# Performance work log

Measured on AMD Instinct MI355X. Metric: run time of the kernel, lower is better.

The kernel has to match this reference:

```python
import jax, jax.numpy as jnp
import numpy as np

D_MODEL = 1024
N_HEAD = 16
B, S = 2, 2048


def setup_inputs() -> dict:
    key = jax.random.key(0)
    ks = jax.random.split(key, 12)
    scale = 1.0 / np.sqrt(D_MODEL)
    inp = {
        "q": jax.random.normal(ks[0], (B, S, D_MODEL), jnp.float32),
        "k": jax.random.normal(ks[1], (B, S, D_MODEL), jnp.float32),
        "v": jax.random.normal(ks[2], (B, S, D_MODEL), jnp.float32),
        "mask": jax.random.randint(ks[3], (B, S, S), 0, 2, jnp.int32),
        "Wq": jax.random.normal(ks[4], (D_MODEL, D_MODEL), jnp.float32) * scale,
        "bq": jnp.zeros((D_MODEL,), jnp.float32),
        "Wk": jax.random.normal(ks[5], (D_MODEL, D_MODEL), jnp.float32) * scale,
        "bk": jnp.zeros((D_MODEL,), jnp.float32),
        "Wv": jax.random.normal(ks[6], (D_MODEL, D_MODEL), jnp.float32) * scale,
        "bv": jnp.zeros((D_MODEL,), jnp.float32),
        "Wo": jax.random.normal(ks[7], (D_MODEL, D_MODEL), jnp.float32) * scale,
        "bo": jnp.zeros((D_MODEL,), jnp.float32),
    }
    return inp


def reference(q, k, v, mask, Wq, bq, Wk, bk, Wv, bv, Wo, bo):
    b, s, d = q.shape
    dh = d // N_HEAD

    def proj_split(x, W, bias):
        # torch nn.Linear: x @ W.T + b; then split to [b, h, s, dh]
        y = x @ W.T + bias
        return y.reshape(b, s, N_HEAD, dh).transpose(0, 2, 1, 3)

    qh = proj_split(q, Wq, bq)
    kh = proj_split(k, Wk, bk)
    vh = proj_split(v, Wv, bv)

    # score: [b, h, s_q, s_k]
    score = jnp.einsum("bhqd,bhkd->bhqk", qh, kh) / jnp.sqrt(jnp.float32(dh))
    score = jnp.where(mask[:, None, :, :] == 0, jnp.float32(-10000.0), score)
    attn = jax.nn.softmax(score, axis=-1)

    out = jnp.einsum("bhqk,bhkd->bhqd", attn, vh)
    out = out.transpose(0, 2, 1, 3).reshape(b, s, d)
    return out @ Wo.T + bo
```

## Files before the change

### kernel.cpp

```cpp
#include <hip/hip_runtime.h>

typedef unsigned short u16;
typedef __bf16 bf16x8 __attribute__((ext_vector_type(8)));
typedef float f32x4 __attribute__((ext_vector_type(4)));

#define D_MODEL 1024
#define NH 16
#define DH 64
#define BB 2
#define SS 2048

#if __has_builtin(__builtin_amdgcn_exp2f)
#define EXP2f(x) __builtin_amdgcn_exp2f(x)
#else
#define EXP2f(x) exp2f(x)
#endif

__device__ __forceinline__ u16 f2bf_fast(float f) {
    union { float f; unsigned int u; } v; v.f = f;
    return (u16)((v.u + 0x8000u) >> 16);
}
__device__ __forceinline__ uint4 pack8(const float4& a, const float4& b) {
    unsigned int a0 = __float_as_uint(a.x) + 0x8000u, a1 = __float_as_uint(a.y) + 0x8000u;
    unsigned int a2 = __float_as_uint(a.z) + 0x8000u, a3 = __float_as_uint(a.w) + 0x8000u;
    unsigned int b0 = __float_as_uint(b.x) + 0x8000u, b1 = __float_as_uint(b.y) + 0x8000u;
    unsigned int b2 = __float_as_uint(b.z) + 0x8000u, b3 = __float_as_uint(b.w) + 0x8000u;
    uint4 r;
    r.x = __builtin_amdgcn_perm(a1, a0, 0x07060302);
    r.y = __builtin_amdgcn_perm(a3, a2, 0x07060302);
    r.z = __builtin_amdgcn_perm(b1, b0, 0x07060302);
    r.w = __builtin_amdgcn_perm(b3, b2, 0x07060302);
    return r;
}

__device__ __forceinline__ void gld16(const void* g, void* l) {
    __builtin_amdgcn_global_load_lds(
        (const __attribute__((address_space(1))) unsigned int*)g,
        (__attribute__((address_space(3))) unsigned int*)l, 16, 0, 0);
}

__global__ __launch_bounds__(256) void cvtw_kernel(
    const float* __restrict__ Wq, const float* __restrict__ Wk,
    const float* __restrict__ Wv, const float* __restrict__ Wo, u16* __restrict__ cW)
{
    int z = blockIdx.y;
    const float* src = (z == 0) ? Wq : (z == 1) ? Wk : (z == 2) ? Wv : Wo;
    u16* dst = cW + (size_t)z * D_MODEL * D_MODEL;
    size_t base = ((size_t)blockIdx.x * 256 + threadIdx.x) * 8;
    float4 a = *reinterpret_cast<const float4*>(src + base);
    float4 b = *reinterpret_cast<const float4*>(src + base + 4);
    *reinterpret_cast<uint4*>(dst + base) = pack8(a, b);
}

__global__ __launch_bounds__(256) void cvtin_kernel(
    const float* __restrict__ q, const float* __restrict__ k,
    const float* __restrict__ v, u16* __restrict__ qb)
{
    int z = blockIdx.y;
    const float* src = (z == 0) ? q : (z == 1) ? k : v;
    u16* dst = qb + (size_t)z * BB * SS * D_MODEL;
    size_t base = ((size_t)blockIdx.x * 256 + threadIdx.x) * 8;
    float4 a = *reinterpret_cast<const float4*>(src + base);
    float4 b = *reinterpret_cast<const float4*>(src + base + 4);
    *reinterpret_cast<uint4*>(dst + base) = pack8(a, b);
}

__global__ __launch_bounds__(256) void maskpack_kernel(
    const int* __restrict__ mask, unsigned long long* __restrict__ pm)
{
    int gw = (blockIdx.x * 256 + threadIdx.x) >> 6;
    int l = threadIdx.x & 63;
#pragma unroll 4
    for (int i = 0; i < 32; ++i) {
        int widx = gw * 32 + i;
        int m = mask[(size_t)widx * 64 + l];
        unsigned long long bits = __ballot(m != 0);
        if (l == 0) pm[widx] = bits;
    }
}

template<int OF32, int QKV>
__device__ void gemm_bb(const u16* __restrict__ A, const u16* __restrict__ W,
                        const float* __restrict__ bias, void* outp, float oscale)
{
    __shared__ __align__(16) u16 smem[128 * 144];
    u16* lA = smem;
    u16* lW = smem + 128 * 64;
    const int t = threadIdx.x, w = t >> 6, l = t & 63;
    const int blockM = blockIdx.x * 128, blockN = blockIdx.y * 128;
    const int lrow = l >> 3, lcol = (l & 7) * 8;
    const int quad = l >> 4, c16 = l & 15;

    f32x4 acc[4][4] = {};

    for (int kt = 0; kt < 16; ++kt) {
        __syncthreads();
#pragma unroll
        for (int i = 0; i < 4; ++i) {
            int c = w * 4 + i;
            int row = c * 8 + lrow;
            gld16(A + (size_t)(blockM + row) * 1024 + kt * 64 + lcol, &lA[c * 512]);
            gld16(W + (size_t)(blockN + row) * 1024 + kt * 64 + lcol, &lW[c * 512]);
        }
        __syncthreads();
#pragma unroll
        for (int ks = 0; ks < 2; ++ks) {
            bf16x8 af[4], bfr[4];
#pragma unroll
            for (int mi = 0; mi < 4; ++mi)
                af[mi] = *reinterpret_cast<const bf16x8*>(
                    &lA[((w & 1) * 64 + mi * 16 + c16) * 64 + ks * 32 + quad * 8]);
#pragma unroll
            for (int ni = 0; ni < 4; ++ni)
                bfr[ni] = *reinterpret_cast<const bf16x8*>(
                    &lW[((w >> 1) * 64 + ni * 16 + c16) * 64 + ks * 32 + quad * 8]);
#pragma unroll
            for (int mi = 0; mi < 4; ++mi)
#pragma unroll
                for (int ni = 0; ni < 4; ++ni)
                    acc[mi][ni] = __builtin_amdgcn_mfma_f32_16x16x32_bf16(
                        af[mi], bfr[ni], acc[mi][ni], 0, 0, 0);
        }
    }

    if (QKV) {
        __syncthreads();
        const int m_base = (w & 1) * 64, n_base = (w >> 1) * 64;
#pragma unroll
        for (int ni = 0; ni < 4; ++ni) {
            int n_local = n_base + ni * 16 + c16;
            float bv = bias[blockN + n_local];
#pragma unroll
            for (int mi = 0; mi < 4; ++mi)
#pragma unroll
                for (int r = 0; r < 4; ++r) {
                    int m_local = m_base + mi * 16 + quad * 4 + r;
                    smem[m_local * 136 + n_local] =
                        f2bf_fast((acc[mi][ni][r] + bv) * oscale);
                }
        }
        __syncthreads();
        const int bb = blockM >> 11, s_base = blockM & 2047;
        u16* outb = (u16*)outp;
#pragma unroll
        for (int i = 0; i < 8; ++i) {
            int idx = t + i * 256;
            int mrow = idx >> 4, ch = idx & 15;
            uint4 val = *reinterpret_cast<const uint4*>(&smem[mrow * 136 + ch * 8]);
            int gn = blockN + ch * 8;
            int hh = gn >> 6, dh = gn & 63;
            *reinterpret_cast<uint4*>(
                outb + (((size_t)(bb * NH + hh)) * SS + s_base + mrow) * DH + dh) = val;
        }
        return;
    }

    const int m0 = blockM + (w & 1) * 64, n0 = blockN + (w >> 1) * 64;
#pragma unroll
    for (int ni = 0; ni < 4; ++ni) {
        int n = n0 + ni * 16 + c16;
        float bv = bias[n];
#pragma unroll
        for (int mi = 0; mi < 4; ++mi) {
#pragma unroll
            for (int r = 0; r < 4; ++r) {
                int m = m0 + mi * 16 + quad * 4 + r;
                float val = (acc[mi][ni][r] + bv) * oscale;
                ((float*)outp)[(size_t)m * 1024 + n] = val;
            }
        }
    }
}

__global__ __launch_bounds__(256) void qkv_kernel(
    const u16* __restrict__ qb, const u16* __restrict__ cW,
    const float* __restrict__ bq, const float* __restrict__ bk, const float* __restrict__ bv,
    u16* __restrict__ qh, u16* __restrict__ kh, u16* __restrict__ vh)
{
    int z = blockIdx.z;
    const u16* A = qb + (size_t)z * BB * SS * D_MODEL;
    const u16* W = cW + (size_t)z * D_MODEL * D_MODEL;
    const float* bias = (z == 0) ? bq : (z == 1) ? bk : bv;
    u16* out = (z == 0) ? qh : (z == 1) ? kh : vh;
    float oscale = (z == 0) ? 0.18033688011112042f : 1.0f;
    gemm_bb<0, 1>(A, W, bias, out, oscale);
}

__global__ __launch_bounds__(256) void oproj_kernel(
    const u16* __restrict__ A, const u16* __restrict__ cWo,
    const float* __restrict__ bo, float* __restrict__ out)
{
    gemm_bb<1, 0>(A, cWo, bo, out, 1.0f);
}

__global__ __launch_bounds__(256, 2) void attn_kernel(
    const u16* __restrict__ qh, const u16* __restrict__ kh, const u16* __restrict__ vh,
    const unsigned long long* __restrict__ pm, u16* __restrict__ ao)
{
    __shared__ __align__(16) u16 lK[64 * 72];
    __shared__ __align__(16) u16 lVt[64 * 72];
    __shared__ __align__(16) u16 lP[128 * 72];

    const int t = threadIdx.x, w = t >> 6, l = t & 63;
    const int qt = blockIdx.x, h = blockIdx.y, b = blockIdx.z;
    const int sq0 = qt * 128;
    const size_t headbase = ((size_t)(b * NH + h)) * SS * DH;
    const int quad = l >> 4, c16 = l & 15;
    const int lrow = l >> 3, lcol = (l & 7) * 8;
    const int vd2 = t & 31, vg = t >> 5;

#pragma unroll
    for (int i = 0; i < 4; ++i) {
        int row = (w * 4 + i) * 8 + lrow;
        uint4 rq = *reinterpret_cast<const uint4*>(
            qh + headbase + (size_t)(sq0 + row) * DH + lcol);
        *reinterpret_cast<uint4*>(&lP[row * 72 + lcol]) = rq;
    }
    __asm__ volatile("s_waitcnt lgkmcnt(0)" ::: "memory");
    bf16x8 qf[2][2];
#pragma unroll
    for (int g = 0; g < 2; ++g)
#pragma unroll
        for (int ks = 0; ks < 2; ++ks)
            qf[g][ks] = *reinterpret_cast<const bf16x8*>(
                &lP[(w * 32 + g * 16 + c16) * 72 + ks * 32 + quad * 8]);

    f32x4 oAcc[2][4] = {};
    float rsumAcc[2] = {0.f, 0.f};
    const size_t pmrow0 = ((size_t)b * SS + sq0 + w * 32 + c16) * 32;
    const size_t pmrow1 = pmrow0 + 16 * 32;

    uint4 rk[2];
    unsigned int rvv[8];
    unsigned long long mw_cur0, mw_cur1, mw_next0, mw_next1;
#pragma unroll
    for (int i = 0; i < 2; ++i) {
        int row = (w * 2 + i) * 8 + lrow;
        rk[i] = *reinterpret_cast<const uint4*>(kh + headbase + (size_t)row * DH + lcol);
    }
#pragma unroll
    for (int e = 0; e < 8; ++e)
        rvv[e] = *reinterpret_cast<const unsigned int*>(
            vh + headbase + (size_t)(vg * 8 + e) * DH + vd2 * 2);
    mw_cur0 = pm[pmrow0 + 0];
    mw_cur1 = pm[pmrow1 + 0];

    for (int kt = 0; kt < 32; ++kt) {
        __syncthreads();
#pragma unroll
        for (int i = 0; i < 2; ++i) {
            int row = (w * 2 + i) * 8 + lrow;
            *reinterpret_cast<uint4*>(&lK[row * 72 + lcol]) = rk[i];
        }
        {
            uint4 cA, cB;
            cA.x = __builtin_amdgcn_perm(rvv[1], rvv[0], 0x05040100);
            cA.y = __builtin_amdgcn_perm(rvv[3], rvv[2], 0x05040100);
            cA.z = __builtin_amdgcn_perm(rvv[5], rvv[4], 0x05040100);
            cA.w = __builtin_amdgcn_perm(rvv[7], rvv[6], 0x05040100);
            cB.x = __builtin_amdgcn_perm(rvv[1], rvv[0], 0x07060302);
            cB.y = __builtin_amdgcn_perm(rvv[3], rvv[2], 0x07060302);
            cB.z = __builtin_amdgcn_perm(rvv[5], rvv[4], 0x07060302);
            cB.w = __builtin_amdgcn_perm(rvv[7], rvv[6], 0x07060302);
            *reinterpret_cast<uint4*>(&lVt[(2 * vd2) * 72 + vg * 8]) = cA;
            *reinterpret_cast<uint4*>(&lVt[(2 * vd2 + 1) * 72 + vg * 8]) = cB;
        }
        __syncthreads();
        {
            int ktn = (kt < 31) ? kt + 1 : kt;
            const int sk0n = ktn * 64;
#pragma unroll
            for (int i = 0; i < 2; ++i) {
                int row = (w * 2 + i) * 8 + lrow;
                rk[i] = *reinterpret_cast<const uint4*>(
                    kh + headbase + (size_t)(sk0n + row) * DH + lcol);
            }
#pragma unroll
            for (int e = 0; e < 8; ++e)
                rvv[e] = *reinterpret_cast<const unsigned int*>(
                    vh + headbase + (size_t)(sk0n + vg * 8 + e) * DH + vd2 * 2);
            mw_next0 = pm[pmrow0 + ktn];
            mw_next1 = pm[pmrow1 + ktn];
        }

        f32x4 sAcc[2][4] = {};
        __builtin_amdgcn_s_setprio(1);
#pragma unroll
        for (int ks = 0; ks < 2; ++ks) {
#pragma unroll
            for (int ni = 0; ni < 4; ++ni) {
                bf16x8 kf = *reinterpret_cast<const bf16x8*>(
                    &lK[(ni * 16 + c16) * 72 + ks * 32 + quad * 8]);
                sAcc[0][ni] = __builtin_amdgcn_mfma_f32_16x16x32_bf16(
                    kf, qf[0][ks], sAcc[0][ni], 0, 0, 0);
                sAcc[1][ni] = __builtin_amdgcn_mfma_f32_16x16x32_bf16(
                    kf, qf[1][ks], sAcc[1][ni], 0, 0, 0);
            }
        }
        __builtin_amdgcn_s_setprio(0);

#pragma unroll
        for (int g = 0; g < 2; ++g) {
            unsigned long long mw = g ? mw_cur1 : mw_cur0;
            unsigned long long mq = mw >> (quad * 4);
            unsigned int mlo = (unsigned int)mq, mhi = (unsigned int)(mq >> 32);
            float rs = 0.f;
#pragma unroll
            for (int ni = 0; ni < 4; ++ni) {
                unsigned int half = (ni < 2) ? mlo : mhi;
                unsigned int sh = (ni & 1) * 16;
                unsigned int w0, w1;
                {
                    float p0 = ((half >> (sh + 0)) & 1u) ? EXP2f(sAcc[g][ni][0]) : 0.f;
                    float p1 = ((half >> (sh + 1)) & 1u) ? EXP2f(sAcc[g][ni][1]) : 0.f;
                    float p2 = ((half >> (sh + 2)) & 1u) ? EXP2f(sAcc[g][ni][2]) : 0.f;
                    float p3 = ((half >> (sh + 3)) & 1u) ? EXP2f(sAcc[g][ni][3]) : 0.f;
                    rs += (p0 + p1) + (p2 + p3);
                    w0 = __builtin_amdgcn_perm(__float_as_uint(p1) + 0x8000u,
                                               __float_as_uint(p0) + 0x8000u, 0x07060302);
                    w1 = __builtin_amdgcn_perm(__float_as_uint(p3) + 0x8000u,
                                               __float_as_uint(p2) + 0x8000u, 0x07060302);
                }
                uint2 pv; pv.x = w0; pv.y = w1;
                *reinterpret_cast<uint2*>(
                    &lP[(w * 32 + g * 16 + c16) * 72 + ni * 16 + quad * 4]) = pv;
            }
            if (g == 0) rsumAcc[0] += rs; else rsumAcc[1] += rs;
        }
        mw_cur0 = mw_next0; mw_cur1 = mw_next1;
        __asm__ volatile("s_waitcnt lgkmcnt(0)" ::: "memory");

        __builtin_amdgcn_s_setprio(1);
#pragma unroll
        for (int ks = 0; ks < 2; ++ks) {
            bf16x8 pf0 = *reinterpret_cast<const bf16x8*>(
                &lP[(w * 32 + c16) * 72 + ks * 32 + quad * 8]);
            bf16x8 pf1 = *reinterpret_cast<const bf16x8*>(
                &lP[(w * 32 + 16 + c16) * 72 + ks * 32 + quad * 8]);
#pragma unroll
            for (int no = 0; no < 4; ++no) {
                bf16x8 vf = *reinterpret_cast<const bf16x8*>(
                    &lVt[(no * 16 + c16) * 72 + ks * 32 + quad * 8]);
                oAcc[0][no] = __builtin_amdgcn_mfma_f32_16x16x32_bf16(
                    pf0, vf, oAcc[0][no], 0, 0, 0);
                oAcc[1][no] = __builtin_amdgcn_mfma_f32_16x16x32_bf16(
                    pf1, vf, oAcc[1][no], 0, 0, 0);
            }
        }
        __builtin_amdgcn_s_setprio(0);
    }

    float linv[2][4];
#pragma unroll
    for (int g = 0; g < 2; ++g) {
        float s = (g == 0) ? rsumAcc[0] : rsumAcc[1];
        s += __shfl_xor(s, 16);
        s += __shfl_xor(s, 32);
        float rinv = 1.0f / s;
#pragma unroll
        for (int r = 0; r < 4; ++r)
            linv[g][r] = __shfl(rinv, quad * 4 + r);
    }
#pragma unroll
    for (int g = 0; g < 2; ++g)
#pragma unroll
        for (int no = 0; no < 4; ++no)
#pragma unroll
            for (int r = 0; r < 4; ++r)
                lP[(w * 32 + g * 16 + quad * 4 + r) * 72 + no * 16 + c16] =
                    f2bf_fast(oAcc[g][no][r] * linv[g][r]);
    __syncthreads();
#pragma unroll
    for (int i = 0; i < 4; ++i) {
        int idx = t + i * 256;
        int row = idx >> 3, ch = idx & 7;
        uint4 val = *reinterpret_cast<const uint4*>(&lP[row * 72 + ch * 8]);
        *reinterpret_cast<uint4*>(
            ao + ((size_t)b * SS + sq0 + row) * D_MODEL + h * DH + ch * 8) = val;
    }
}

extern "C" void kernel_launch(void* const* d_in, const int* in_sizes, int n_in,
                              void* d_out, int out_size, void* d_ws, size_t ws_size,
                              hipStream_t stream)
{
    const float* q    = (const float*)d_in[0];
    const float* k    = (const float*)d_in[1];
    const float* v    = (const float*)d_in[2];
    const int*   mask = (const int*)d_in[3];
    const float* Wq   = (const float*)d_in[4];
    const float* bq   = (const float*)d_in[5];
    const float* Wk   = (const float*)d_in[6];
    const float* bk   = (const float*)d_in[7];
    const float* Wv   = (const float*)d_in[8];
    const float* bv   = (const float*)d_in[9];
    const float* Wo   = (const float*)d_in[10];
    const float* bo   = (const float*)d_in[11];

    const size_t T4M = (size_t)BB * SS * D_MODEL;
    u16* qh = (u16*)d_ws;
    u16* kh = qh + T4M;
    u16* vh = kh + T4M;
    u16* ao = vh + T4M;
    u16* cW = ao + T4M;
    u16* qb = cW + 4 * (size_t)D_MODEL * D_MODEL;
    unsigned long long* pm = (unsigned long long*)(qb + 3 * T4M);
    float* out = (float*)d_out;

    cvtw_kernel<<<dim3(512, 4), 256, 0, stream>>>(Wq, Wk, Wv, Wo, cW);
    cvtin_kernel<<<dim3(2048, 3), 256, 0, stream>>>(q, k, v, qb);
    maskpack_kernel<<<1024, 256, 0, stream>>>(mask, pm);
    qkv_kernel<<<dim3(32, 8, 3), 256, 0, stream>>>(qb, cW, bq, bk, bv, qh, kh, vh);
    attn_kernel<<<dim3(16, NH, BB), 256, 0, stream>>>(qh, kh, vh, pm, ao);
    oproj_kernel<<<dim3(32, 8), 256, 0, stream>>>(ao, cW + 3 * (size_t)D_MODEL * D_MODEL, bo, out);
}
```

Baseline: 303.7 us.

## Fuse fp32-to-bf16 input conversion into QKV GEMM and merge prep kernels

```diff
diff --git a/kernel.cpp b/kernel.cpp
--- a/kernel.cpp
+++ b/kernel.cpp
@@ -39,49 +39,36 @@
         (__attribute__((address_space(3))) unsigned int*)l, 16, 0, 0);
 }
 
-__global__ __launch_bounds__(256) void cvtw_kernel(
+__global__ __launch_bounds__(256) void prep_kernel(
     const float* __restrict__ Wq, const float* __restrict__ Wk,
-    const float* __restrict__ Wv, const float* __restrict__ Wo, u16* __restrict__ cW)
-{
-    int z = blockIdx.y;
-    const float* src = (z == 0) ? Wq : (z == 1) ? Wk : (z == 2) ? Wv : Wo;
-    u16* dst = cW + (size_t)z * D_MODEL * D_MODEL;
-    size_t base = ((size_t)blockIdx.x * 256 + threadIdx.x) * 8;
-    float4 a = *reinterpret_cast<const float4*>(src + base);
-    float4 b = *reinterpret_cast<const float4*>(src + base + 4);
-    *reinterpret_cast<uint4*>(dst + base) = pack8(a, b);
-}
-
-__global__ __launch_bounds__(256) void cvtin_kernel(
-    const float* __restrict__ q, const float* __restrict__ k,
-    const float* __restrict__ v, u16* __restrict__ qb)
-{
-    int z = blockIdx.y;
-    const float* src = (z == 0) ? q : (z == 1) ? k : v;
-    u16* dst = qb + (size_t)z * BB * SS * D_MODEL;
-    size_t base = ((size_t)blockIdx.x * 256 + threadIdx.x) * 8;
-    float4 a = *reinterpret_cast<const float4*>(src + base);
-    float4 b = *reinterpret_cast<const float4*>(src + base + 4);
-    *reinterpret_cast<uint4*>(dst + base) = pack8(a, b);
-}
-
-__global__ __launch_bounds__(256) void maskpack_kernel(
+    const float* __restrict__ Wv, const float* __restrict__ Wo, u16* __restrict__ cW,
     const int* __restrict__ mask, unsigned long long* __restrict__ pm)
 {
-    int gw = (blockIdx.x * 256 + threadIdx.x) >> 6;
-    int l = threadIdx.x & 63;
+    int bid = blockIdx.x;
+    if (bid < 2048) {
+        int z = bid >> 9, x = bid & 511;
+        const float* src = (z == 0) ? Wq : (z == 1) ? Wk : (z == 2) ? Wv : Wo;
+        u16* dst = cW + (size_t)z * D_MODEL * D_MODEL;
+        size_t base = ((size_t)x * 256 + threadIdx.x) * 8;
+        float4 a = *reinterpret_cast<const float4*>(src + base);
+        float4 b = *reinterpret_cast<const float4*>(src + base + 4);
+        *reinterpret_cast<uint4*>(dst + base) = pack8(a, b);
+    } else {
+        int x = bid - 2048;
+        int gw = (x * 256 + threadIdx.x) >> 6;
+        int l = threadIdx.x & 63;
 #pragma unroll 4
-    for (int i = 0; i < 32; ++i) {
-        int widx = gw * 32 + i;
-        int m = mask[(size_t)widx * 64 + l];
-        unsigned long long bits = __ballot(m != 0);
-        if (l == 0) pm[widx] = bits;
-    }
-}
-
-template<int OF32, int QKV>
-__device__ void gemm_bb(const u16* __restrict__ A, const u16* __restrict__ W,
-                        const float* __restrict__ bias, void* outp, float oscale)
+        for (int i = 0; i < 32; ++i) {
+            int widx = gw * 32 + i;
+            int m = mask[(size_t)widx * 64 + l];
+            unsigned long long bits = __ballot(m != 0);
+            if (l == 0) pm[widx] = bits;
+        }
+    }
+}
+
+__device__ void gemm_bb_f32out(const u16* __restrict__ A, const u16* __restrict__ W,
+                               const float* __restrict__ bias, float* outp, float oscale)
 {
     __shared__ __align__(16) u16 smem[128 * 144];
     u16* lA = smem;
@@ -123,38 +110,6 @@
         }
     }
 
-    if (QKV) {
-        __syncthreads();
-        const int m_base = (w & 1) * 64, n_base = (w >> 1) * 64;
-#pragma unroll
-        for (int ni = 0; ni < 4; ++ni) {
-            int n_local = n_base + ni * 16 + c16;
-            float bv = bias[blockN + n_local];
-#pragma unroll
-            for (int mi = 0; mi < 4; ++mi)
-#pragma unroll
-                for (int r = 0; r < 4; ++r) {
-                    int m_local = m_base + mi * 16 + quad * 4 + r;
-                    smem[m_local * 136 + n_local] =
-                        f2bf_fast((acc[mi][ni][r] + bv) * oscale);
-                }
-        }
-        __syncthreads();
-        const int bb = blockM >> 11, s_base = blockM & 2047;
-        u16* outb = (u16*)outp;
-#pragma unroll
-        for (int i = 0; i < 8; ++i) {
-            int idx = t + i * 256;
-            int mrow = idx >> 4, ch = idx & 15;
-            uint4 val = *reinterpret_cast<const uint4*>(&smem[mrow * 136 + ch * 8]);
-            int gn = blockN + ch * 8;
-            int hh = gn >> 6, dh = gn & 63;
-            *reinterpret_cast<uint4*>(
-                outb + (((size_t)(bb * NH + hh)) * SS + s_base + mrow) * DH + dh) = val;
-        }
-        return;
-    }
-
     const int m0 = blockM + (w & 1) * 64, n0 = blockN + (w >> 1) * 64;
 #pragma unroll
     for (int ni = 0; ni < 4; ++ni) {
@@ -166,31 +121,118 @@
             for (int r = 0; r < 4; ++r) {
                 int m = m0 + mi * 16 + quad * 4 + r;
                 float val = (acc[mi][ni][r] + bv) * oscale;
-                ((float*)outp)[(size_t)m * 1024 + n] = val;
-            }
-        }
+                outp[(size_t)m * 1024 + n] = val;
+            }
+        }
+    }
+}
+
+__device__ void gemm_qkv(const float* __restrict__ A, const u16* __restrict__ W,
+                         const float* __restrict__ bias, u16* __restrict__ outp,
+                         float oscale)
+{
+    __shared__ __align__(16) u16 smem[128 * 144];
+    u16* lA = smem;
+    u16* lW = smem + 128 * 64;
+    const int t = threadIdx.x, w = t >> 6, l = t & 63;
+    const int blockM = blockIdx.x * 128, blockN = blockIdx.y * 128;
+    const int lrow = l >> 3, lcol = (l & 7) * 8;
+    const int quad = l >> 4, c16 = l & 15;
+
+    f32x4 acc[4][4] = {};
+
+    for (int kt = 0; kt < 16; ++kt) {
+        __syncthreads();
+        float4 fa[4][2];
+#pragma unroll
+        for (int i = 0; i < 4; ++i) {
+            int c = w * 4 + i;
+            int row = c * 8 + lrow;
+            const float* srcA = A + (size_t)(blockM + row) * 1024 + kt * 64 + lcol;
+            fa[i][0] = *reinterpret_cast<const float4*>(srcA);
+            fa[i][1] = *reinterpret_cast<const float4*>(srcA + 4);
+        }
+#pragma unroll
+        for (int i = 0; i < 4; ++i) {
+            int c = w * 4 + i;
+            int row = c * 8 + lrow;
+            gld16(W + (size_t)(blockN + row) * 1024 + kt * 64 + lcol, &lW[c * 512]);
+        }
+#pragma unroll
+        for (int i = 0; i < 4; ++i) {
+            int c = w * 4 + i;
+            *reinterpret_cast<uint4*>(&lA[c * 512 + l * 8]) = pack8(fa[i][0], fa[i][1]);
+        }
+        __syncthreads();
+#pragma unroll
+        for (int ks = 0; ks < 2; ++ks) {
+            bf16x8 af[4], bfr[4];
+#pragma unroll
+            for (int mi = 0; mi < 4; ++mi)
+                af[mi] = *reinterpret_cast<const bf16x8*>(
+                    &lA[((w & 1) * 64 + mi * 16 + c16) * 64 + ks * 32 + quad * 8]);
+#pragma unroll
+            for (int ni = 0; ni < 4; ++ni)
+                bfr[ni] = *reinterpret_cast<const bf16x8*>(
+                    &lW[((w >> 1) * 64 + ni * 16 + c16) * 64 + ks * 32 + quad * 8]);
+#pragma unroll
+            for (int mi = 0; mi < 4; ++mi)
+#pragma unroll
+                for (int ni = 0; ni < 4; ++ni)
+                    acc[mi][ni] = __builtin_amdgcn_mfma_f32_16x16x32_bf16(
+                        af[mi], bfr[ni], acc[mi][ni], 0, 0, 0);
+        }
+    }
+
+    __syncthreads();
+    const int m_base = (w & 1) * 64, n_base = (w >> 1) * 64;
+#pragma unroll
+    for (int ni = 0; ni < 4; ++ni) {
+        int n_local = n_base + ni * 16 + c16;
+        float bv = bias[blockN + n_local];
+#pragma unroll
+        for (int mi = 0; mi < 4; ++mi)
+#pragma unroll
+            for (int r = 0; r < 4; ++r) {
+                int m_local = m_base + mi * 16 + quad * 4 + r;
+                smem[m_local * 136 + n_local] =
+                    f2bf_fast((acc[mi][ni][r] + bv) * oscale);
+            }
+    }
+    __syncthreads();
+    const int bb = blockM >> 11, s_base = blockM & 2047;
+#pragma unroll
+    for (int i = 0; i < 8; ++i) {
+        int idx = t + i * 256;
+        int mrow = idx >> 4, ch = idx & 15;
+        uint4 val = *reinterpret_cast<const uint4*>(&smem[mrow * 136 + ch * 8]);
+        int gn = blockN + ch * 8;
+        int hh = gn >> 6, dh = gn & 63;
+        *reinterpret_cast<uint4*>(
+            outp + (((size_t)(bb * NH + hh)) * SS + s_base + mrow) * DH + dh) = val;
     }
 }
 
 __global__ __launch_bounds__(256) void qkv_kernel(
-    const u16* __restrict__ qb, const u16* __restrict__ cW,
+    const float* __restrict__ q, const float* __restrict__ k, const float* __restrict__ v,
+    const u16* __restrict__ cW,
     const float* __restrict__ bq, const float* __restrict__ bk, const float* __restrict__ bv,
     u16* __restrict__ qh, u16* __restrict__ kh, u16* __restrict__ vh)
 {
     int z = blockIdx.z;
-    const u16* A = qb + (size_t)z * BB * SS * D_MODEL;
+    const float* A = (z == 0) ? q : (z == 1) ? k : v;
     const u16* W = cW + (size_t)z * D_MODEL * D_MODEL;
     const float* bias = (z == 0) ? bq : (z == 1) ? bk : bv;
     u16* out = (z == 0) ? qh : (z == 1) ? kh : vh;
     float oscale = (z == 0) ? 0.18033688011112042f : 1.0f;
-    gemm_bb<0, 1>(A, W, bias, out, oscale);
+    gemm_qkv(A, W, bias, out, oscale);
 }
 
 __global__ __launch_bounds__(256) void oproj_kernel(
     const u16* __restrict__ A, const u16* __restrict__ cWo,
     const float* __restrict__ bo, float* __restrict__ out)
 {
-    gemm_bb<1, 0>(A, cWo, bo, out, 1.0f);
+    gemm_bb_f32out(A, cWo, bo, out, 1.0f);
 }
 
 __global__ __launch_bounds__(256, 2) void attn_kernel(
@@ -403,14 +445,11 @@
     u16* vh = kh + T4M;
     u16* ao = vh + T4M;
     u16* cW = ao + T4M;
-    u16* qb = cW + 4 * (size_t)D_MODEL * D_MODEL;
-    unsigned long long* pm = (unsigned long long*)(qb + 3 * T4M);
+    unsigned long long* pm = (unsigned long long*)(cW + 4 * (size_t)D_MODEL * D_MODEL);
     float* out = (float*)d_out;
 
-    cvtw_kernel<<<dim3(512, 4), 256, 0, stream>>>(Wq, Wk, Wv, Wo, cW);
-    cvtin_kernel<<<dim3(2048, 3), 256, 0, stream>>>(q, k, v, qb);
-    maskpack_kernel<<<1024, 256, 0, stream>>>(mask, pm);
-    qkv_kernel<<<dim3(32, 8, 3), 256, 0, stream>>>(qb, cW, bq, bk, bv, qh, kh, vh);
+    prep_kernel<<<3072, 256, 0, stream>>>(Wq, Wk, Wv, Wo, cW, mask, pm);
+    qkv_kernel<<<dim3(32, 8, 3), 256, 0, stream>>>(q, k, v, cW, bq, bk, bv, qh, kh, vh);
     attn_kernel<<<dim3(16, NH, BB), 256, 0, stream>>>(qh, kh, vh, pm, ao);
     oproj_kernel<<<dim3(32, 8), 256, 0, stream>>>(ao, cW + 3 * (size_t)D_MODEL * D_MODEL, bo, out);
 }
```

Measured after the change: 311.0 us. 2.4% more time.

## Fuse prep kernels into one launch and store K/V tiles in fragment-native LDS layout

Applied to the files above, without the earlier changes.

```diff
diff --git a/kernel.cpp b/kernel.cpp
--- a/kernel.cpp
+++ b/kernel.cpp
@@ -39,43 +39,42 @@
         (__attribute__((address_space(3))) unsigned int*)l, 16, 0, 0);
 }
 
-__global__ __launch_bounds__(256) void cvtw_kernel(
+__global__ __launch_bounds__(256) void prep_kernel(
     const float* __restrict__ Wq, const float* __restrict__ Wk,
-    const float* __restrict__ Wv, const float* __restrict__ Wo, u16* __restrict__ cW)
-{
-    int z = blockIdx.y;
-    const float* src = (z == 0) ? Wq : (z == 1) ? Wk : (z == 2) ? Wv : Wo;
-    u16* dst = cW + (size_t)z * D_MODEL * D_MODEL;
-    size_t base = ((size_t)blockIdx.x * 256 + threadIdx.x) * 8;
-    float4 a = *reinterpret_cast<const float4*>(src + base);
-    float4 b = *reinterpret_cast<const float4*>(src + base + 4);
-    *reinterpret_cast<uint4*>(dst + base) = pack8(a, b);
-}
-
-__global__ __launch_bounds__(256) void cvtin_kernel(
+    const float* __restrict__ Wv, const float* __restrict__ Wo, u16* __restrict__ cW,
     const float* __restrict__ q, const float* __restrict__ k,
-    const float* __restrict__ v, u16* __restrict__ qb)
-{
-    int z = blockIdx.y;
-    const float* src = (z == 0) ? q : (z == 1) ? k : v;
-    u16* dst = qb + (size_t)z * BB * SS * D_MODEL;
-    size_t base = ((size_t)blockIdx.x * 256 + threadIdx.x) * 8;
-    float4 a = *reinterpret_cast<const float4*>(src + base);
-    float4 b = *reinterpret_cast<const float4*>(src + base + 4);
-    *reinterpret_cast<uint4*>(dst + base) = pack8(a, b);
-}
-
-__global__ __launch_bounds__(256) void maskpack_kernel(
+    const float* __restrict__ v, u16* __restrict__ qb,
     const int* __restrict__ mask, unsigned long long* __restrict__ pm)
 {
-    int gw = (blockIdx.x * 256 + threadIdx.x) >> 6;
-    int l = threadIdx.x & 63;
+    int bid = blockIdx.x;
+    if (bid < 2048) {
+        int z = bid >> 9, x = bid & 511;
+        const float* src = (z == 0) ? Wq : (z == 1) ? Wk : (z == 2) ? Wv : Wo;
+        u16* dst = cW + (size_t)z * D_MODEL * D_MODEL;
+        size_t base = ((size_t)x * 256 + threadIdx.x) * 8;
+        float4 a = *reinterpret_cast<const float4*>(src + base);
+        float4 b = *reinterpret_cast<const float4*>(src + base + 4);
+        *reinterpret_cast<uint4*>(dst + base) = pack8(a, b);
+    } else if (bid < 8192) {
+        int x = bid - 2048;
+        int z = x >> 11, xx = x & 2047;
+        const float* src = (z == 0) ? q : (z == 1) ? k : v;
+        u16* dst = qb + (size_t)z * BB * SS * D_MODEL;
+        size_t base = ((size_t)xx * 256 + threadIdx.x) * 8;
+        float4 a = *reinterpret_cast<const float4*>(src + base);
+        float4 b = *reinterpret_cast<const float4*>(src + base + 4);
+        *reinterpret_cast<uint4*>(dst + base) = pack8(a, b);
+    } else {
+        int x = bid - 8192;
+        int gw = (x * 256 + threadIdx.x) >> 6;
+        int l = threadIdx.x & 63;
 #pragma unroll 4
-    for (int i = 0; i < 32; ++i) {
-        int widx = gw * 32 + i;
-        int m = mask[(size_t)widx * 64 + l];
-        unsigned long long bits = __ballot(m != 0);
-        if (l == 0) pm[widx] = bits;
+        for (int i = 0; i < 32; ++i) {
+            int widx = gw * 32 + i;
+            int m = mask[(size_t)widx * 64 + l];
+            unsigned long long bits = __ballot(m != 0);
+            if (l == 0) pm[widx] = bits;
+        }
     }
 }
 
@@ -197,8 +196,8 @@
     const u16* __restrict__ qh, const u16* __restrict__ kh, const u16* __restrict__ vh,
     const unsigned long long* __restrict__ pm, u16* __restrict__ ao)
 {
-    __shared__ __align__(16) u16 lK[64 * 72];
-    __shared__ __align__(16) u16 lVt[64 * 72];
+    __shared__ __align__(16) u16 lK[8 * 512];
+    __shared__ __align__(16) u16 lVt[8 * 512];
     __shared__ __align__(16) u16 lP[128 * 72];
 
     const int t = threadIdx.x, w = t >> 6, l = t & 63;
@@ -230,13 +229,16 @@
     const size_t pmrow0 = ((size_t)b * SS + sq0 + w * 32 + c16) * 32;
     const size_t pmrow1 = pmrow0 + 16 * 32;
 
+    const int kcol = quad * 8;
+
     uint4 rk[2];
     unsigned int rvv[8];
     unsigned long long mw_cur0, mw_cur1, mw_next0, mw_next1;
 #pragma unroll
     for (int i = 0; i < 2; ++i) {
-        int row = (w * 2 + i) * 8 + lrow;
-        rk[i] = *reinterpret_cast<const uint4*>(kh + headbase + (size_t)row * DH + lcol);
+        int c = w * 2 + i;
+        rk[i] = *reinterpret_cast<const uint4*>(
+            kh + headbase + (size_t)((c >> 1) * 16 + c16) * DH + (c & 1) * 32 + kcol);
     }
 #pragma unroll
     for (int e = 0; e < 8; ++e)
@@ -245,13 +247,14 @@
     mw_cur0 = pm[pmrow0 + 0];
     mw_cur1 = pm[pmrow1 + 0];
 
+    const int vchunk = (vd2 >> 3) * 2 + (vg >> 2);
+    const int vlane = (vg & 3) * 16 + ((2 * vd2) & 15);
+
     for (int kt = 0; kt < 32; ++kt) {
         __syncthreads();
 #pragma unroll
-        for (int i = 0; i < 2; ++i) {
-            int row = (w * 2 + i) * 8 + lrow;
-            *reinterpret_cast<uint4*>(&lK[row * 72 + lcol]) = rk[i];
-        }
+        for (int i = 0; i < 2; ++i)
+            *reinterpret_cast<uint4*>(&lK[(w * 2 + i) * 512 + l * 8]) = rk[i];
         {
             uint4 cA, cB;
             cA.x = __builtin_amdgcn_perm(rvv[1], rvv[0], 0x05040100);
@@ -262,8 +265,9 @@
             cB.y = __builtin_amdgcn_perm(rvv[3], rvv[2], 0x07060302);
             cB.z = __builtin_amdgcn_perm(rvv[5], rvv[4], 0x07060302);
             cB.w = __builtin_amdgcn_perm(rvv[7], rvv[6], 0x07060302);
-            *reinterpret_cast<uint4*>(&lVt[(2 * vd2) * 72 + vg * 8]) = cA;
-            *reinterpret_cast<uint4*>(&lVt[(2 * vd2 + 1) * 72 + vg * 8]) = cB;
+            u16* vdst = &lVt[vchunk * 512 + vlane * 8];
+            *reinterpret_cast<uint4*>(vdst) = cA;
+            *reinterpret_cast<uint4*>(vdst + 8) = cB;
         }
         __syncthreads();
         {
@@ -271,9 +275,10 @@
             const int sk0n = ktn * 64;
 #pragma unroll
             for (int i = 0; i < 2; ++i) {
-                int row = (w * 2 + i) * 8 + lrow;
+                int c = w * 2 + i;
                 rk[i] = *reinterpret_cast<const uint4*>(
-                    kh + headbase + (size_t)(sk0n + row) * DH + lcol);
+                    kh + headbase + (size_t)(sk0n + (c >> 1) * 16 + c16) * DH +
+                    (c & 1) * 32 + kcol);
             }
 #pragma unroll
             for (int e = 0; e < 8; ++e)
@@ -290,7 +295,7 @@
 #pragma unroll
             for (int ni = 0; ni < 4; ++ni) {
                 bf16x8 kf = *reinterpret_cast<const bf16x8*>(
-                    &lK[(ni * 16 + c16) * 72 + ks * 32 + quad * 8]);
+                    &lK[(ni * 2 + ks) * 512 + l * 8]);
                 sAcc[0][ni] = __builtin_amdgcn_mfma_f32_16x16x32_bf16(
                     kf, qf[0][ks], sAcc[0][ni], 0, 0, 0);
                 sAcc[1][ni] = __builtin_amdgcn_mfma_f32_16x16x32_bf16(
@@ -340,7 +345,7 @@
 #pragma unroll
             for (int no = 0; no < 4; ++no) {
                 bf16x8 vf = *reinterpret_cast<const bf16x8*>(
-                    &lVt[(no * 16 + c16) * 72 + ks * 32 + quad * 8]);
+                    &lVt[(no * 2 + ks) * 512 + l * 8]);
                 oAcc[0][no] = __builtin_amdgcn_mfma_f32_16x16x32_bf16(
                     pf0, vf, oAcc[0][no], 0, 0, 0);
                 oAcc[1][no] = __builtin_amdgcn_mfma_f32_16x16x32_bf16(
@@ -407,9 +412,7 @@
     unsigned long long* pm = (unsigned long long*)(qb + 3 * T4M);
     float* out = (float*)d_out;
 
-    cvtw_kernel<<<dim3(512, 4), 256, 0, stream>>>(Wq, Wk, Wv, Wo, cW);
-    cvtin_kernel<<<dim3(2048, 3), 256, 0, stream>>>(q, k, v, qb);
-    maskpack_kernel<<<1024, 256, 0, stream>>>(mask, pm);
+    prep_kernel<<<9216, 256, 0, stream>>>(Wq, Wk, Wv, Wo, cW, q, k, v, qb, mask, pm);
     qkv_kernel<<<dim3(32, 8, 3), 256, 0, stream>>>(qb, cW, bq, bk, bv, qh, kh, vh);
     attn_kernel<<<dim3(16, NH, BB), 256, 0, stream>>>(qh, kh, vh, pm, ao);
     oproj_kernel<<<dim3(32, 8), 256, 0, stream>>>(ao, cW + 3 * (size_t)D_MODEL * D_MODEL, bo, out);
```

Measured after the change: 302.5 us. About the same (-0.4%).
